# Optimization experiments

Hardware: AMD Instinct MI355X
Metric: run time of the kernel (lower is better)

## Reference

```python
import jax, jax.numpy as jnp
import numpy as np

TANH_CONST = 1.5  # tanh_constant in __init__
EPS = 1e-9


def setup_inputs() -> dict:
    key = jax.random.key(0)
    ks = jax.random.split(key, 6)
    B, H, NOPS, T = 8192, 100, 5, 512
    return {
        "x0": jax.random.uniform(ks[0], (B, H), dtype=jnp.float32),          # g_emb-style uniform start input
        "W_x": jax.random.normal(ks[1], (H, 4 * H), dtype=jnp.float32) * 0.1,  # LSTMCell kernel (no bias)
        "W_h": jax.random.normal(ks[2], (H, 4 * H), dtype=jnp.float32) * 0.1,  # LSTMCell recurrent kernel
        "W_ops": jax.random.normal(ks[3], (H, NOPS), dtype=jnp.float32) * 0.1, # dense_ops (no bias)
        "emb": jax.random.normal(ks[4], (NOPS + 1, H), dtype=jnp.float32),     # Embedding(num_ops+1, lstm_size)
        "u": jax.random.uniform(ks[5], (T, B, NOPS), dtype=jnp.float32),       # uniform noise -> Gumbel-max sampling
    }


def reference(x0, W_x, W_h, W_ops, emb, u):
    # Gumbel noise for categorical sampling (equiv. in distribution to tf.random.categorical)
    g = -jnp.log(-jnp.log(u + EPS) + EPS)  # [T, B, num_ops]
    B, H = x0.shape

    def step(carry, g_t):
        h, c, x = carry
        # Keras LSTMCell, use_bias=False: gate order (i, f, c, o)
        z = x @ W_x + h @ W_h                      # [B, 4H]
        zi, zf, zc, zo = jnp.split(z, 4, axis=-1)
        c_new = jax.nn.sigmoid(zf) * c + jax.nn.sigmoid(zi) * jnp.tanh(zc)
        h_new = jax.nn.sigmoid(zo) * jnp.tanh(c_new)
        logits = TANH_CONST * jnp.tanh(h_new @ W_ops)  # tanh_constant * tanh(dense_ops(h))
        op = jnp.argmax(logits + g_t, axis=-1)         # [B] sampled op ids
        logp = jax.nn.log_softmax(logits, axis=-1)
        cur = -jnp.take_along_axis(logp, op[:, None], axis=-1)[:, 0]  # sparse xent vs sampled label
        ent = jax.lax.stop_gradient(cur * jnp.exp(-cur))
        x_new = emb[op]                                # next-step input = embedding(op_id)
        return (h_new, c_new, x_new), (cur, ent, op)

    h0 = jnp.zeros((B, H), x0.dtype)
    c0 = jnp.zeros((B, H), x0.dtype)
    _, (curs, ents, ops) = jax.lax.scan(step, (h0, c0, x0), g)
    log_prob = curs.sum(0)   # [B] accumulated self.log_prob
    entropy = ents.sum(0)    # [B] accumulated self.entropy
    return log_prob, entropy, ops
```

## Files before the change

kernel.cpp:

```cpp
#include <hip/hip_runtime.h>
#include <cstdint>
#include <cstddef>

typedef __attribute__((ext_vector_type(8))) short short8;
typedef __attribute__((ext_vector_type(4))) short bfx4;
typedef __attribute__((ext_vector_type(4))) float f32x4;

#define HH     100
#define G4     400
#define NCOL   416
#define NTIL   26
#define KTN    3
#define KRES   96
#define BTOT   8192
#define TST    512
#define ROWS   32
#define NBLK   256
#define BLOCK  832
#define ZW     420
#define TANHC  1.5f
#define EPSF   1e-9f

__device__ unsigned short d_Bhi[NTIL*KTN*64*8];
__device__ unsigned short d_Blo[NTIL*KTN*64*8];
__device__ float d_Ep2[6*G4];
__device__ float d_WresG[NCOL*4];
__device__ float d_Z0[(size_t)BTOT*G4];

static __device__ __forceinline__ unsigned short bf16hi(float f){
  unsigned u = __float_as_uint(f);
  return (unsigned short)((u + 0x7FFFu + ((u>>16)&1u)) >> 16);
}
static __device__ __forceinline__ float bf16f(unsigned short s){
  return __uint_as_float(((unsigned)s)<<16);
}
static __device__ __forceinline__ float frcp(float x){ return __builtin_amdgcn_rcpf(x); }
static __device__ __forceinline__ float sigf(float x){ return frcp(1.0f + __expf(-x)); }
static __device__ __forceinline__ float tanh_f(float x){ return 1.0f - 2.0f*frcp(__expf(2.0f*x) + 1.0f); }


__global__ void setup_bpack(const float* __restrict__ Wh, const float* __restrict__ Wops){
  int idx = blockIdx.x*blockDim.x + threadIdx.x;
  if (idx >= NTIL*KTN*64) return;
  int tile = idx/(KTN*64), rem = idx - tile*(KTN*64), kt = rem>>6, ln = rem&63;
  int n = tile*16 + (ln & 15);
  #pragma unroll
  for (int i = 0; i < 8; ++i){
    int k = kt*32 + (ln>>4)*8 + i;
    float w = 0.f;
    if (n < G4)          w = Wh[k*G4 + n];
    else if (n < G4+5)   w = Wops[k*5 + (n - G4)];
    unsigned short hi = bf16hi(w);
    unsigned short lo = bf16hi(w - bf16f(hi));
    d_Bhi[idx*8+i] = hi;
    d_Blo[idx*8+i] = lo;
  }
}

__global__ void setup_misc(const float* __restrict__ emb, const float* __restrict__ Wx,
                           const float* __restrict__ Wh, const float* __restrict__ Wops){
  int idx = blockIdx.x*blockDim.x + threadIdx.x;
  if (idx < 6*G4){
    int e = idx/G4, r2 = idx - e*G4, je = r2>>2, g = r2&3;
    float s = 0.f;
    for (int k = 0; k < HH; ++k) s = fmaf(emb[e*HH+k], Wx[k*G4 + g*HH + je], s);
    d_Ep2[idx] = s;
  } else if (idx < 6*G4 + NCOL*4){
    int i = idx - 6*G4, n = i>>2, q = i&3;
    float w = 0.f;
    if (n < G4)        w = Wh[(KRES+q)*G4 + n];
    else if (n < G4+5) w = Wops[(KRES+q)*5 + (n - G4)];
    d_WresG[i] = w;
  }
}

__global__ __launch_bounds__(256) void setup_z0(const float* __restrict__ x0,
                                                const float* __restrict__ Wx){
  __shared__ float xs[64*101];
  const int bb = blockIdx.x * 64;
  for (int i = threadIdx.x; i < 64*HH; i += 256){
    int r = i/HH, k = i - r*HH;
    xs[r*101 + k] = x0[(size_t)(bb + r)*HH + k];
  }
  __syncthreads();
  const int bl = threadIdx.x & 63;
  for (int ng = threadIdx.x >> 6; ng < HH; ng += 4){
    f32x4 a = {0.f,0.f,0.f,0.f};
    for (int k = 0; k < HH; ++k){
      f32x4 w = *(const f32x4*)&Wx[k*G4 + ng*4];
      a += w * xs[bl*101 + k];
    }
    *(f32x4*)&d_Z0[(size_t)(bb + bl)*G4 + ng*4] = a;
  }
}


__global__ __launch_bounds__(BLOCK) void rnn_main(
    const float* __restrict__ u, float* __restrict__ out)
{
  __shared__ __align__(16) float z_lds[ROWS*ZW];
  __shared__ __align__(16) unsigned short fhi[2*KTN*64*8];
  __shared__ __align__(16) unsigned short flo[2*KTN*64*8];
  __shared__ __align__(16) float h_res[4*ROWS];
  __shared__ __align__(16) float Ep2_l[6*G4];
  __shared__ __align__(16) float Wres_l[NCOL*4];
  __shared__ __align__(16) float samp[5*36];
  __shared__ __align__(16) float gn_lds[ROWS*5];
  __shared__ int op_lds[ROWS];

  const int tid  = threadIdx.x;
  const int wave = tid >> 6;
  const int lane = tid & 63;
  const int cn   = lane & 15;
  const int q4   = lane >> 4;
  const int row0 = blockIdx.x * ROWS;
  const int jg   = tid >> 5;
  const int rE   = tid & 31;

  for (int i = tid; i < 6*G4;   i += BLOCK) Ep2_l[i]  = d_Ep2[i];
  for (int i = tid; i < NCOL*4; i += BLOCK) Wres_l[i] = d_WresG[i];

  short8 bh[2][KTN], bl[2][KTN];
  {
    const short8* bph = (const short8*)d_Bhi;
    const short8* bpl = (const short8*)d_Blo;
    #pragma unroll
    for (int tl = 0; tl < 2; ++tl)
      #pragma unroll
      for (int kt = 0; kt < KTN; ++kt){
        int fi = ((wave*2 + tl)*KTN + kt)*64 + lane;
        bh[tl][kt] = bph[fi];
        bl[tl][kt] = bpl[fi];
      }
  }

  float c_st[4] = {0.f,0.f,0.f,0.f};
  float lp_acc = 0.f, ent_acc = 0.f;

  for (int t = 0; t <= TST; ++t){
    if (t == 0){
      if (tid < 800){
        #pragma unroll
        for (int i = 0; i < 4; ++i){
          f32x4 v = *(const f32x4*)&d_Z0[(size_t)(row0 + rE)*G4 + jg*16 + i*4];
          *(f32x4*)&z_lds[rE*ZW + jg*16 + i*4] = v;
        }
      }
    } else {
      #pragma unroll
      for (int mt = 0; mt < 2; ++mt){
        short8 ah[KTN], al[KTN];
        #pragma unroll
        for (int kt = 0; kt < KTN; ++kt){
          ah[kt] = *(const short8*)&fhi[((mt*KTN + kt)*64 + lane)*8];
          al[kt] = *(const short8*)&flo[((mt*KTN + kt)*64 + lane)*8];
        }
        f32x4 hq[4];
        #pragma unroll
        for (int q = 0; q < 4; ++q)
          hq[q] = *(const f32x4*)&h_res[q*ROWS + mt*16 + q4*4];
        #pragma unroll
        for (int tl = 0; tl < 2; ++tl){
          const int n = (wave*2 + tl)*16 + cn;
          f32x4 acc = {0.f,0.f,0.f,0.f};
          #pragma unroll
          for (int kt = 0; kt < KTN; ++kt){
            acc = __builtin_amdgcn_mfma_f32_16x16x32_bf16(ah[kt], bh[tl][kt], acc, 0,0,0);
            acc = __builtin_amdgcn_mfma_f32_16x16x32_bf16(al[kt], bh[tl][kt], acc, 0,0,0);
            acc = __builtin_amdgcn_mfma_f32_16x16x32_bf16(ah[kt], bl[tl][kt], acc, 0,0,0);
            acc = __builtin_amdgcn_mfma_f32_16x16x32_bf16(al[kt], bl[tl][kt], acc, 0,0,0);
          }
          f32x4 wr = *(const f32x4*)&Wres_l[n*4];
          #pragma unroll
          for (int q = 0; q < 4; ++q) acc += hq[q] * wr[q];
          const int rowb = mt*16 + q4*4;
          #pragma unroll
          for (int i = 0; i < 4; ++i)
            z_lds[(rowb + i)*ZW + n] = acc[i];
          if (wave == 12 && tl == 1 && cn < 5)
            *(f32x4*)&samp[cn*36 + mt*16 + q4*4] = acc;
        }
      }
      if (wave == 12 && lane < 32){
        int r = lane;
        float l[5];
        #pragma unroll
        for (int o = 0; o < 5; ++o) l[o] = TANHC * tanh_f(samp[o*36 + r]);
        int op = 0; float best = -1e30f;
        #pragma unroll
        for (int o = 0; o < 5; ++o){
          float v = l[o] + gn_lds[r*5 + o];
          if (v > best){ best = v; op = o; }
        }
        float mx = fmaxf(fmaxf(fmaxf(l[0],l[1]), fmaxf(l[2],l[3])), l[4]);
        float se = 0.f;
        #pragma unroll
        for (int o = 0; o < 5; ++o) se += __expf(l[o] - mx);
        float lse = mx + __logf(se);
        float cur = lse - l[op];
        lp_acc  += cur;
        ent_acc += cur * __expf(-cur);
        op_lds[r] = op;
        out[2*BTOT + (size_t)(t-1)*BTOT + row0 + r] = (float)op;
      }
    }
    if (t == TST) break;
    __syncthreads();

    if (tid < 800){
      f32x4 zg[4];
      #pragma unroll
      for (int g = 0; g < 4; ++g)
        zg[g] = *(const f32x4*)&z_lds[rE*ZW + g*HH + jg*4];
      if (t > 0){
        const int op = op_lds[rE];
        #pragma unroll
        for (int i = 0; i < 4; ++i){
          f32x4 e4 = *(const f32x4*)&Ep2_l[op*G4 + (jg*4 + i)*4];
          zg[0][i] += e4.x; zg[1][i] += e4.y; zg[2][i] += e4.z; zg[3][i] += e4.w;
        }
      }
      float hv[4];
      #pragma unroll
      for (int i = 0; i < 4; ++i){
        float cn_ = sigf(zg[1][i])*c_st[i] + sigf(zg[0][i])*tanh_f(zg[2][i]);
        c_st[i] = cn_;
        hv[i] = sigf(zg[3][i])*tanh_f(cn_);
      }
      if (jg < 24){
        bfx4 h4, l4;
        #pragma unroll
        for (int i = 0; i < 4; ++i){
          unsigned short hi = bf16hi(hv[i]);
          h4[i] = (short)hi;
          l4[i] = (short)bf16hi(hv[i] - bf16f(hi));
        }
        const int kt   = jg >> 3;
        const int lf   = (rE & 15) | (((jg >> 1) & 3) << 4);
        const int mt   = rE >> 4;
        const int j0   = (jg & 1) * 4;
        const int base = ((mt*KTN + kt)*64 + lf)*8 + j0;
        *(bfx4*)&fhi[base] = h4;
        *(bfx4*)&flo[base] = l4;
      } else {
        #pragma unroll
        for (int i = 0; i < 4; ++i) h_res[i*ROWS + rE] = hv[i];
      }
    } else {
      int r = tid - 800;
      const float* up = u + ((size_t)t*BTOT + row0 + r)*5;
      #pragma unroll
      for (int o = 0; o < 5; ++o){
        float uu = up[o];
        gn_lds[r*5 + o] = -__logf(-__logf(uu + EPSF) + EPSF);
      }
    }
    __syncthreads();
  }

  if (wave == 12 && lane < 32){
    out[row0 + lane]        = lp_acc;
    out[BTOT + row0 + lane] = ent_acc;
  }
}

extern "C" void kernel_launch(void* const* d_in, const int* in_sizes, int n_in,
                              void* d_out, int out_size, void* d_ws, size_t ws_size,
                              hipStream_t stream) {
  const float* x0   = (const float*)d_in[0];
  const float* Wx   = (const float*)d_in[1];
  const float* Wh   = (const float*)d_in[2];
  const float* Wops = (const float*)d_in[3];
  const float* emb  = (const float*)d_in[4];
  const float* u    = (const float*)d_in[5];
  (void)d_ws; (void)ws_size; (void)in_sizes; (void)n_in;

  setup_bpack<<<(NTIL*KTN*64 + 255)/256, 256, 0, stream>>>(Wh, Wops);
  setup_misc<<<(6*G4 + NCOL*4 + 255)/256, 256, 0, stream>>>(emb, Wx, Wh, Wops);
  setup_z0<<<BTOT/64, 256, 0, stream>>>(x0, Wx);
  rnn_main<<<NBLK, BLOCK, 0, stream>>>(u, (float*)d_out);
}
```

Measured before the change: 2.281 ms.

## Halve rows per block to 16 and prefetch noise loads early

Cuts the batch rows per workgroup from 32 to 16 and doubles the block count to 512, so each block runs one MFMA M-tile per step instead of two and the per-step serial chain gets shorter. This also spreads the work over more CUs on the MI355X. The elementwise LSTM update now uses 400 threads, so the other threads sit idle. The uniform-noise loads are moved to the top of each step so their latency overlaps the MFMA phase. In exchange, each block still loads the full weight fragments, so weight traffic per row doubles and many threads do nothing.

```diff
diff --git a/kernel.cpp b/kernel.cpp
--- a/kernel.cpp
+++ b/kernel.cpp
@@ -14,8 +14,8 @@
 #define KRES   96
 #define BTOT   8192
 #define TST    512
-#define ROWS   32
-#define NBLK   256
+#define ROWS   16
+#define NBLK   512
 #define BLOCK  832
 #define ZW     420
 #define TANHC  1.5f
@@ -99,12 +99,12 @@
     const float* __restrict__ u, float* __restrict__ out)
 {
   __shared__ __align__(16) float z_lds[ROWS*ZW];
-  __shared__ __align__(16) unsigned short fhi[2*KTN*64*8];
-  __shared__ __align__(16) unsigned short flo[2*KTN*64*8];
+  __shared__ __align__(16) unsigned short fhi[KTN*64*8];
+  __shared__ __align__(16) unsigned short flo[KTN*64*8];
   __shared__ __align__(16) float h_res[4*ROWS];
   __shared__ __align__(16) float Ep2_l[6*G4];
   __shared__ __align__(16) float Wres_l[NCOL*4];
-  __shared__ __align__(16) float samp[5*36];
+  __shared__ __align__(16) float samp[5*20];
   __shared__ __align__(16) float gn_lds[ROWS*5];
   __shared__ int op_lds[ROWS];
 
@@ -114,8 +114,8 @@
   const int cn   = lane & 15;
   const int q4   = lane >> 4;
   const int row0 = blockIdx.x * ROWS;
-  const int jg   = tid >> 5;
-  const int rE   = tid & 31;
+  const int jg   = tid >> 4;
+  const int rE   = tid & 15;
 
   for (int i = tid; i < 6*G4;   i += BLOCK) Ep2_l[i]  = d_Ep2[i];
   for (int i = tid; i < NCOL*4; i += BLOCK) Wres_l[i] = d_WresG[i];
@@ -138,8 +138,15 @@
   float lp_acc = 0.f, ent_acc = 0.f;
 
   for (int t = 0; t <= TST; ++t){
+    float upr[5];
+    if (t < TST && tid >= 800 && tid < 816){
+      const float* up = u + ((size_t)t*BTOT + row0 + (tid - 800))*5;
+      #pragma unroll
+      for (int o = 0; o < 5; ++o) upr[o] = up[o];
+    }
+
     if (t == 0){
-      if (tid < 800){
+      if (tid < 400){
         #pragma unroll
         for (int i = 0; i < 4; ++i){
           f32x4 v = *(const f32x4*)&d_Z0[(size_t)(row0 + rE)*G4 + jg*16 + i*4];
@@ -147,45 +154,42 @@
         }
       }
     } else {
-      #pragma unroll
-      for (int mt = 0; mt < 2; ++mt){
-        short8 ah[KTN], al[KTN];
+      short8 ah[KTN], al[KTN];
+      #pragma unroll
+      for (int kt = 0; kt < KTN; ++kt){
+        ah[kt] = *(const short8*)&fhi[(kt*64 + lane)*8];
+        al[kt] = *(const short8*)&flo[(kt*64 + lane)*8];
+      }
+      f32x4 hq[4];
+      #pragma unroll
+      for (int q = 0; q < 4; ++q)
+        hq[q] = *(const f32x4*)&h_res[q*ROWS + q4*4];
+      #pragma unroll
+      for (int tl = 0; tl < 2; ++tl){
+        const int n = (wave*2 + tl)*16 + cn;
+        f32x4 acc = {0.f,0.f,0.f,0.f};
         #pragma unroll
         for (int kt = 0; kt < KTN; ++kt){
-          ah[kt] = *(const short8*)&fhi[((mt*KTN + kt)*64 + lane)*8];
-          al[kt] = *(const short8*)&flo[((mt*KTN + kt)*64 + lane)*8];
-        }
-        f32x4 hq[4];
-        #pragma unroll
-        for (int q = 0; q < 4; ++q)
-          hq[q] = *(const f32x4*)&h_res[q*ROWS + mt*16 + q4*4];
-        #pragma unroll
-        for (int tl = 0; tl < 2; ++tl){
-          const int n = (wave*2 + tl)*16 + cn;
-          f32x4 acc = {0.f,0.f,0.f,0.f};
-          #pragma unroll
-          for (int kt = 0; kt < KTN; ++kt){
-            acc = __builtin_amdgcn_mfma_f32_16x16x32_bf16(ah[kt], bh[tl][kt], acc, 0,0,0);
-            acc = __builtin_amdgcn_mfma_f32_16x16x32_bf16(al[kt], bh[tl][kt], acc, 0,0,0);
-            acc = __builtin_amdgcn_mfma_f32_16x16x32_bf16(ah[kt], bl[tl][kt], acc, 0,0,0);
-            acc = __builtin_amdgcn_mfma_f32_16x16x32_bf16(al[kt], bl[tl][kt], acc, 0,0,0);
-          }
-          f32x4 wr = *(const f32x4*)&Wres_l[n*4];
-          #pragma unroll
-          for (int q = 0; q < 4; ++q) acc += hq[q] * wr[q];
-          const int rowb = mt*16 + q4*4;
-          #pragma unroll
-          for (int i = 0; i < 4; ++i)
-            z_lds[(rowb + i)*ZW + n] = acc[i];
-          if (wave == 12 && tl == 1 && cn < 5)
-            *(f32x4*)&samp[cn*36 + mt*16 + q4*4] = acc;
-        }
-      }
-      if (wave == 12 && lane < 32){
+          acc = __builtin_amdgcn_mfma_f32_16x16x32_bf16(ah[kt], bh[tl][kt], acc, 0,0,0);
+          acc = __builtin_amdgcn_mfma_f32_16x16x32_bf16(al[kt], bh[tl][kt], acc, 0,0,0);
+          acc = __builtin_amdgcn_mfma_f32_16x16x32_bf16(ah[kt], bl[tl][kt], acc, 0,0,0);
+          acc = __builtin_amdgcn_mfma_f32_16x16x32_bf16(al[kt], bl[tl][kt], acc, 0,0,0);
+        }
+        f32x4 wr = *(const f32x4*)&Wres_l[n*4];
+        #pragma unroll
+        for (int q = 0; q < 4; ++q) acc += hq[q] * wr[q];
+        const int rowb = q4*4;
+        #pragma unroll
+        for (int i = 0; i < 4; ++i)
+          z_lds[(rowb + i)*ZW + n] = acc[i];
+        if (wave == 12 && tl == 1 && cn < 5)
+          *(f32x4*)&samp[cn*20 + q4*4] = acc;
+      }
+      if (wave == 12 && lane < 16){
         int r = lane;
         float l[5];
         #pragma unroll
-        for (int o = 0; o < 5; ++o) l[o] = TANHC * tanh_f(samp[o*36 + r]);
+        for (int o = 0; o < 5; ++o) l[o] = TANHC * tanh_f(samp[o*20 + r]);
         int op = 0; float best = -1e30f;
         #pragma unroll
         for (int o = 0; o < 5; ++o){
@@ -207,7 +211,7 @@
     if (t == TST) break;
     __syncthreads();
 
-    if (tid < 800){
+    if (tid < 400){
       f32x4 zg[4];
       #pragma unroll
       for (int g = 0; g < 4; ++g)
@@ -236,29 +240,25 @@
           l4[i] = (short)bf16hi(hv[i] - bf16f(hi));
         }
         const int kt   = jg >> 3;
-        const int lf   = (rE & 15) | (((jg >> 1) & 3) << 4);
-        const int mt   = rE >> 4;
+        const int lf   = rE | (((jg >> 1) & 3) << 4);
         const int j0   = (jg & 1) * 4;
-        const int base = ((mt*KTN + kt)*64 + lf)*8 + j0;
+        const int base = (kt*64 + lf)*8 + j0;
         *(bfx4*)&fhi[base] = h4;
         *(bfx4*)&flo[base] = l4;
       } else {
         #pragma unroll
         for (int i = 0; i < 4; ++i) h_res[i*ROWS + rE] = hv[i];
       }
-    } else {
+    } else if (tid >= 800 && tid < 816){
       int r = tid - 800;
-      const float* up = u + ((size_t)t*BTOT + row0 + r)*5;
-      #pragma unroll
-      for (int o = 0; o < 5; ++o){
-        float uu = up[o];
-        gn_lds[r*5 + o] = -__logf(-__logf(uu + EPSF) + EPSF);
-      }
+      #pragma unroll
+      for (int o = 0; o < 5; ++o)
+        gn_lds[r*5 + o] = -__logf(-__logf(upr[o] + EPSF) + EPSF);
     }
     __syncthreads();
   }
 
-  if (wave == 12 && lane < 32){
+  if (wave == 12 && lane < 16){
     out[row0 + lane]        = lp_acc;
     out[BTOT + row0 + lane] = ent_acc;
   }
```

After: 2.407 ms. 1.06x slower.

## Shrink RNN block to 512 threads with uneven tile split and prefetched noise

Applied to the files above, without the earlier changes.

Cuts the main recurrent kernel from 13 waves to 8 and spreads the 26 MFMA column tiles unevenly (3 or 4 per wave). Each thread now runs one or two LSTM cell-update slots, keeping two cell states. The Gumbel noise load is issued at the start of each step so its latency hides behind the MFMA phase. With launch_bounds(512,2), this aims to lower barrier cost and allow two blocks per CU, but each wave does more serial work, which may lengthen the per-step critical path.

```diff
diff --git a/kernel.cpp b/kernel.cpp
--- a/kernel.cpp
+++ b/kernel.cpp
@@ -16,7 +16,7 @@
 #define TST    512
 #define ROWS   32
 #define NBLK   256
-#define BLOCK  832
+#define BLOCK  512
 #define ZW     420
 #define TANHC  1.5f
 #define EPSF   1e-9f
@@ -95,7 +95,7 @@
 }
 
 
-__global__ __launch_bounds__(BLOCK) void rnn_main(
+__global__ __launch_bounds__(BLOCK, 2) void rnn_main(
     const float* __restrict__ u, float* __restrict__ out)
 {
   __shared__ __align__(16) float z_lds[ROWS*ZW];
@@ -114,37 +114,44 @@
   const int cn   = lane & 15;
   const int q4   = lane >> 4;
   const int row0 = blockIdx.x * ROWS;
-  const int jg   = tid >> 5;
   const int rE   = tid & 31;
 
   for (int i = tid; i < 6*G4;   i += BLOCK) Ep2_l[i]  = d_Ep2[i];
   for (int i = tid; i < NCOL*4; i += BLOCK) Wres_l[i] = d_WresG[i];
 
-  short8 bh[2][KTN], bl[2][KTN];
+  const int tb  = (wave==0) ? 23 : (wave < 6) ? 3*(wave-1) : 15 + 4*(wave-6);
+  const int ntl = (wave >= 6) ? 4 : 3;
+  short8 bh[4][KTN], bl[4][KTN];
   {
     const short8* bph = (const short8*)d_Bhi;
     const short8* bpl = (const short8*)d_Blo;
     #pragma unroll
-    for (int tl = 0; tl < 2; ++tl)
+    for (int tl = 0; tl < 4; ++tl) if (tl < ntl)
       #pragma unroll
       for (int kt = 0; kt < KTN; ++kt){
-        int fi = ((wave*2 + tl)*KTN + kt)*64 + lane;
+        int fi = ((tb+tl)*KTN + kt)*64 + lane;
         bh[tl][kt] = bph[fi];
         bl[tl][kt] = bpl[fi];
       }
   }
 
-  float c_st[4] = {0.f,0.f,0.f,0.f};
+  float cs1[4] = {0.f,0.f,0.f,0.f};
+  float cs2[4] = {0.f,0.f,0.f,0.f};
   float lp_acc = 0.f, ent_acc = 0.f;
 
   for (int t = 0; t <= TST; ++t){
+    float upr[5];
+    if (t < TST && tid >= 416 && tid < 448){
+      const float* up = u + ((size_t)t*BTOT + row0 + (tid - 416))*5;
+      #pragma unroll
+      for (int o = 0; o < 5; ++o) upr[o] = up[o];
+    }
+
     if (t == 0){
-      if (tid < 800){
-        #pragma unroll
-        for (int i = 0; i < 4; ++i){
-          f32x4 v = *(const f32x4*)&d_Z0[(size_t)(row0 + rE)*G4 + jg*16 + i*4];
-          *(f32x4*)&z_lds[rE*ZW + jg*16 + i*4] = v;
-        }
+      for (int i = tid; i < ROWS*HH; i += BLOCK){
+        int r = i/HH, c4 = i - r*HH;
+        *(f32x4*)&z_lds[r*ZW + c4*4] =
+          *(const f32x4*)&d_Z0[(size_t)(row0 + r)*G4 + c4*4];
       }
     } else {
       #pragma unroll
@@ -160,8 +167,8 @@
         for (int q = 0; q < 4; ++q)
           hq[q] = *(const f32x4*)&h_res[q*ROWS + mt*16 + q4*4];
         #pragma unroll
-        for (int tl = 0; tl < 2; ++tl){
-          const int n = (wave*2 + tl)*16 + cn;
+        for (int tl = 0; tl < 4; ++tl) if (tl < ntl){
+          const int n = (tb+tl)*16 + cn;
           f32x4 acc = {0.f,0.f,0.f,0.f};
           #pragma unroll
           for (int kt = 0; kt < KTN; ++kt){
@@ -177,11 +184,11 @@
           #pragma unroll
           for (int i = 0; i < 4; ++i)
             z_lds[(rowb + i)*ZW + n] = acc[i];
-          if (wave == 12 && tl == 1 && cn < 5)
+          if (wave == 0 && tl == 2 && cn < 5)
             *(f32x4*)&samp[cn*36 + mt*16 + q4*4] = acc;
         }
       }
-      if (wave == 12 && lane < 32){
+      if (wave == 0 && lane < 32){
         int r = lane;
         float l[5];
         #pragma unroll
@@ -207,7 +214,8 @@
     if (t == TST) break;
     __syncthreads();
 
-    if (tid < 800){
+    {
+      const int jg = tid >> 5;
       f32x4 zg[4];
       #pragma unroll
       for (int g = 0; g < 4; ++g)
@@ -223,11 +231,48 @@
       float hv[4];
       #pragma unroll
       for (int i = 0; i < 4; ++i){
-        float cn_ = sigf(zg[1][i])*c_st[i] + sigf(zg[0][i])*tanh_f(zg[2][i]);
-        c_st[i] = cn_;
+        float cn_ = sigf(zg[1][i])*cs1[i] + sigf(zg[0][i])*tanh_f(zg[2][i]);
+        cs1[i] = cn_;
         hv[i] = sigf(zg[3][i])*tanh_f(cn_);
       }
-      if (jg < 24){
+      bfx4 h4, l4;
+      #pragma unroll
+      for (int i = 0; i < 4; ++i){
+        unsigned short hi = bf16hi(hv[i]);
+        h4[i] = (short)hi;
+        l4[i] = (short)bf16hi(hv[i] - bf16f(hi));
+      }
+      const int kt   = jg >> 3;
+      const int lf   = (rE & 15) | (((jg >> 1) & 3) << 4);
+      const int mt   = rE >> 4;
+      const int j0   = (jg & 1) * 4;
+      const int base = ((mt*KTN + kt)*64 + lf)*8 + j0;
+      *(bfx4*)&fhi[base] = h4;
+      *(bfx4*)&flo[base] = l4;
+    }
+    if (tid < 256 || tid >= 480){
+      const int jg = (tid < 256) ? (16 + (tid >> 5)) : 24;
+      const int c0 = jg*4;
+      f32x4 zg[4];
+      #pragma unroll
+      for (int g = 0; g < 4; ++g)
+        zg[g] = *(const f32x4*)&z_lds[rE*ZW + g*HH + c0];
+      if (t > 0){
+        const int op = op_lds[rE];
+        #pragma unroll
+        for (int i = 0; i < 4; ++i){
+          f32x4 e4 = *(const f32x4*)&Ep2_l[op*G4 + (c0 + i)*4];
+          zg[0][i] += e4.x; zg[1][i] += e4.y; zg[2][i] += e4.z; zg[3][i] += e4.w;
+        }
+      }
+      float hv[4];
+      #pragma unroll
+      for (int i = 0; i < 4; ++i){
+        float cn_ = sigf(zg[1][i])*cs2[i] + sigf(zg[0][i])*tanh_f(zg[2][i]);
+        cs2[i] = cn_;
+        hv[i] = sigf(zg[3][i])*tanh_f(cn_);
+      }
+      if (tid < 256){
         bfx4 h4, l4;
         #pragma unroll
         for (int i = 0; i < 4; ++i){
@@ -246,19 +291,16 @@
         #pragma unroll
         for (int i = 0; i < 4; ++i) h_res[i*ROWS + rE] = hv[i];
       }
-    } else {
-      int r = tid - 800;
-      const float* up = u + ((size_t)t*BTOT + row0 + r)*5;
-      #pragma unroll
-      for (int o = 0; o < 5; ++o){
-        float uu = up[o];
-        gn_lds[r*5 + o] = -__logf(-__logf(uu + EPSF) + EPSF);
-      }
+    } else if (tid >= 416 && tid < 448){
+      int r = tid - 416;
+      #pragma unroll
+      for (int o = 0; o < 5; ++o)
+        gn_lds[r*5 + o] = -__logf(-__logf(upr[o] + EPSF) + EPSF);
     }
     __syncthreads();
   }
 
-  if (wave == 12 && lane < 32){
+  if (wave == 0 && lane < 32){
     out[row0 + lane]        = lp_acc;
     out[BTOT + row0 + lane] = ent_acc;
   }
```

Result: faster. 2.081 ms (-8.8%).
